# Kernel tuning notes

Hardware: AMD Instinct MI355X
Metric: run time of the kernel (lower is better)

Reference implementation:

```python
import jax, jax.numpy as jnp
import numpy as np

N, L, C, H, W, HEAD = 16, 256, 512, 32, 32, 16

def setup_inputs() -> dict:
    key = jax.random.key(0)
    ks = jax.random.split(key, 8)
    s = 0.02  # weight init scale
    return {
        "feature": jax.random.normal(ks[0], (N, C, H, W), jnp.float32),
        "token": jax.random.normal(ks[1], (N, L, C), jnp.float32),
        "wq": jax.random.normal(ks[2], (C, C), jnp.float32) * s,
        "bq": jax.random.normal(ks[3], (C,), jnp.float32) * s,
        "wk": jax.random.normal(ks[4], (C, C), jnp.float32) * s,
        "bk": jax.random.normal(ks[5], (C,), jnp.float32) * s,
        "wv": jax.random.normal(ks[6], (C, C), jnp.float32) * s,
        "bv": jax.random.normal(ks[7], (C,), jnp.float32) * s,
    }

def reference(feature, token, wq, bq, wk, bk, wv, bv):
    n, c, hgt, wid = feature.shape
    h = HEAD
    d = c // h
    l = token.shape[1]
    scale = jnp.asarray(np.sqrt(c / h), feature.dtype)
    tok = token.transpose(0, 2, 1)  # (N, C, L)
    # 1x1 conv projections == per-position GEMMs
    v = (jnp.einsum('ncl,dc->ndl', tok, wv) + bv[None, :, None]).reshape(n, h, d, l)
    k = (jnp.einsum('ncl,dc->ndl', tok, wk) + bk[None, :, None]).reshape(n, h, d, l)
    q = (jnp.einsum('nchw,dc->ndhw', feature, wq) + bq[None, :, None, None])
    q = q.reshape(n, h, d, hgt * wid).transpose(0, 1, 3, 2)  # (N, h, HW, d)
    scores = jnp.einsum('nhqd,nhdl->nhql', q, k) / scale  # (N, h, HW, L)
    coef = jax.nn.softmax(scores, axis=-1)
    proj = jnp.einsum('nhdl,nhql->nhdq', v, coef)  # (N, h, d, HW)
    return feature + proj.reshape(n, c, hgt, wid)
```

## Files before the change

### kernel.cpp

```cpp
#include <hip/hip_runtime.h>
#include <hip/hip_bf16.h>

#define N_ 16
#define L_ 256
#define C_ 512
#define HW_ 1024
#define HEADS_ 16
#define DH_ 32

typedef unsigned short u16;
typedef unsigned int u32;
typedef __attribute__((ext_vector_type(8))) short short8_t;
typedef __attribute__((ext_vector_type(4))) float f32x4;

__device__ __forceinline__ u16 f2bs(float f) {
    union { float f; u32 i; } x; x.f = f;
    u32 r = x.i + 0x7fffu + ((x.i >> 16) & 1u);
    return (u16)(r >> 16);
}
__device__ __forceinline__ u32 cvt_pk_bf16(float lo, float hi) {
    u32 r;
    asm("v_cvt_pk_bf16_f32 %0, %1, %2" : "=v"(r) : "v"(lo), "v"(hi));
    return r;
}
__device__ __forceinline__ void cvt8(const float* __restrict__ src, void* dst) {
    float4 lo = *(const float4*)src;
    float4 hi = *(const float4*)(src + 4);
    union { u32 w[4]; short8_t v; } pk;
    pk.w[0] = cvt_pk_bf16(lo.x, lo.y);
    pk.w[1] = cvt_pk_bf16(lo.z, lo.w);
    pk.w[2] = cvt_pk_bf16(hi.x, hi.y);
    pk.w[3] = cvt_pk_bf16(hi.z, hi.w);
    *(short8_t*)dst = pk.v;
}
#define AS1(p) (const __attribute__((address_space(1))) void*)(p)
#define AS3(p) (__attribute__((address_space(3))) void*)(p)

__global__ __launch_bounds__(256) void prep_kernel(
    const float* __restrict__ feature, const float* __restrict__ token,
    const float* __restrict__ wk, const float* __restrict__ wv,
    const float* __restrict__ bk, const float* __restrict__ bv,
    u16* __restrict__ Ftb, u16* __restrict__ Kout, u16* __restrict__ Vt)
{
    __shared__ __align__(16) unsigned char smem[32768];
    const int t = threadIdx.x;

    if (blockIdx.x < 256) {
        const int kvid = blockIdx.x;
        const int xcd = kvid & 7, j = kvid >> 3;
        const int m0 = (xcd * 4 + (j & 3)) * 128;
        const int n0 = (j >> 2) * 64;
        const int lane = t & 63, wid = t >> 6;
        const int i16 = lane & 15, g = lane >> 4;
        const int wm = wid >> 1, wn = wid & 1;
        const int r8 = t >> 3, c8 = t & 7;
        u16* Tok = (u16*)smem;
        u16* Bk  = (u16*)(smem + 16384);
        u16* Bv  = (u16*)(smem + 24576);
        u16 (*LTo)[72] = (u16(*)[72])smem;

        f32x4 ak[4][2], av[4][2];
        #pragma unroll
        for (int mt = 0; mt < 4; ++mt)
            #pragma unroll
            for (int nt = 0; nt < 2; ++nt) {
                ak[mt][nt] = (f32x4){0.f, 0.f, 0.f, 0.f};
                av[mt][nt] = (f32x4){0.f, 0.f, 0.f, 0.f};
            }

        for (int c0 = 0; c0 < C_; c0 += 64) {
            __syncthreads();
            #pragma unroll
            for (int p = 0; p < 4; ++p) {
                const int m = p * 32 + r8;
                cvt8(&token[(size_t)(m0 + m) * C_ + c0 + c8 * 8],
                     &Tok[m * 64 + ((c8 ^ (m & 7)) << 3)]);
            }
            #pragma unroll
            for (int p = 0; p < 2; ++p) {
                const int m = p * 32 + r8;
                const int sw = m * 64 + ((c8 ^ (m & 7)) << 3);
                cvt8(&wk[(size_t)(n0 + m) * C_ + c0 + c8 * 8], &Bk[sw]);
                cvt8(&wv[(size_t)(n0 + m) * C_ + c0 + c8 * 8], &Bv[sw]);
            }
            __syncthreads();
            #pragma unroll
            for (int ks = 0; ks < 2; ++ks) {
                short8_t a[4], bbk[2], bbv[2];
                #pragma unroll
                for (int mt = 0; mt < 4; ++mt) {
                    const int m = wm * 64 + mt * 16 + i16;
                    a[mt] = *(const short8_t*)&Tok[m * 64 + ((((ks << 2) | g) ^ (m & 7)) << 3)];
                }
                #pragma unroll
                for (int nt = 0; nt < 2; ++nt) {
                    const int d = wn * 32 + nt * 16 + i16;
                    const int sw = d * 64 + ((((ks << 2) | g) ^ (d & 7)) << 3);
                    bbk[nt] = *(const short8_t*)&Bk[sw];
                    bbv[nt] = *(const short8_t*)&Bv[sw];
                }
                #pragma unroll
                for (int mt = 0; mt < 4; ++mt)
                    #pragma unroll
                    for (int nt = 0; nt < 2; ++nt) {
                        ak[mt][nt] = __builtin_amdgcn_mfma_f32_16x16x32_bf16(
                            a[mt], bbk[nt], ak[mt][nt], 0, 0, 0);
                        av[mt][nt] = __builtin_amdgcn_mfma_f32_16x16x32_bf16(
                            a[mt], bbv[nt], av[mt][nt], 0, 0, 0);
                    }
            }
        }
        const int nb = m0 >> 8, l0 = m0 & 255;
        const size_t vtbase = (size_t)nb * C_ * L_;
        #pragma unroll
        for (int nt = 0; nt < 2; ++nt) {
            const int d = n0 + wn * 32 + nt * 16 + i16;
            const float bb = bv[d];
            #pragma unroll
            for (int mt = 0; mt < 4; ++mt) {
                ushort4 w;
                w.x = f2bs(av[mt][nt][0] + bb);
                w.y = f2bs(av[mt][nt][1] + bb);
                w.z = f2bs(av[mt][nt][2] + bb);
                w.w = f2bs(av[mt][nt][3] + bb);
                const int l = l0 + wm * 64 + mt * 16 + g * 4;
                *(ushort4*)&Vt[vtbase + (size_t)d * L_ + l] = w;
            }
        }
        __syncthreads();
        #pragma unroll
        for (int nt = 0; nt < 2; ++nt) {
            const int col = wn * 32 + nt * 16 + i16;
            const float bb = bk[n0 + col];
            #pragma unroll
            for (int mt = 0; mt < 4; ++mt)
                #pragma unroll
                for (int r = 0; r < 4; ++r)
                    LTo[wm * 64 + mt * 16 + g * 4 + r][col] = f2bs(ak[mt][nt][r] + bb);
        }
        __syncthreads();
        #pragma unroll
        for (int rep = 0; rep < 4; ++rep) {
            const int m = (t >> 3) + rep * 32;
            const int cs2 = (t & 7) * 8;
            *(short8_t*)&Kout[(size_t)(m0 + m) * C_ + n0 + cs2] = *(short8_t*)&LTo[m][cs2];
        }
    } else {
        float (*LT)[67] = (float(*)[67])smem;
        const int tidx = blockIdx.x - 256;
        const int pb = tidx & 15, cb = (tidx >> 4) & 7, n = tidx >> 7;
        const int c0 = cb * 64, pos0 = pb * 64;

        #pragma unroll
        for (int r = 0; r < 4; ++r) {
            const int c = r * 16 + (t >> 4);
            const int p = (t & 15) * 4;
            float4 v = *(const float4*)&feature[
                ((size_t)n * C_ + c0 + c) * HW_ + pos0 + p];
            LT[c][p] = v.x; LT[c][p+1] = v.y; LT[c][p+2] = v.z; LT[c][p+3] = v.w;
        }
        __syncthreads();
        #pragma unroll
        for (int rep = 0; rep < 2; ++rep) {
            const int pos = (t >> 3) + rep * 32;
            const int c = (t & 7) * 8;
            u16 tmp[8];
            #pragma unroll
            for (int j = 0; j < 8; ++j) tmp[j] = f2bs(LT[c + j][pos]);
            *(short8_t*)&Ftb[(size_t)(n * HW_ + pos0 + pos) * C_ + c0 + c] =
                *(short8_t*)tmp;
        }
    }
}

__global__ __launch_bounds__(256) void fattn_kernel(
    const float* __restrict__ feature, const u16* __restrict__ Ftb,
    const float* __restrict__ wq, const float* __restrict__ bqv,
    const u16* __restrict__ Kws, const u16* __restrict__ Vws,
    float* __restrict__ out)
{
    __shared__ __align__(16) unsigned char smem[32768];
    const u32 QB = 12288;

    const int t = threadIdx.x;
    const int wid = t >> 6, lane = t & 63;
    const int i16 = lane & 15, g = lane >> 4;
    const int h = blockIdx.x & 15;
    const int tile = blockIdx.x >> 4;
    const int n = tile >> 4, pt = tile & 15;
    const int pos0 = pt * 64;
    const size_t kbase = ((size_t)n * L_) * C_ + h * DH_;
    const size_t vbase = (size_t)n * C_ * L_ + (size_t)h * DH_ * L_;
    const size_t fbase = (size_t)(n * HW_ + pos0) * C_;
    const int q = wid * 16 + i16;

    const int r8 = t >> 3, gr = t & 7;
    f32x4 aq0 = {0.f, 0.f, 0.f, 0.f}, aq1 = {0.f, 0.f, 0.f, 0.f};

    #define FQ_STAGE(buf, c0) { \
        _Pragma("unroll") \
        for (int p = 0; p < 2; ++p) { \
            const int row = p * 32 + r8; \
            __builtin_amdgcn_global_load_lds( \
                AS1(Ftb + fbase + (size_t)row * C_ + (c0) + ((gr ^ (row & 7)) << 3)), \
                AS3(smem + (buf) * QB + (p * 32 + wid * 8) * 128), 16, 0, 0); } \
        { \
            const int wrow = t >> 3; \
            float wf[8]; \
            const float* wsrc = wq + (size_t)(h * 32 + wrow) * C_ + (c0) + (t & 7) * 8; \
            *(float4*)&wf[0] = *(const float4*)&wsrc[0]; \
            *(float4*)&wf[4] = *(const float4*)&wsrc[4]; \
            cvt8(wf, smem + (buf) * QB + 8192 + \
                 (u32)(wrow * 128 + (((t & 7) ^ (wrow & 7)) << 4))); \
        } }

    FQ_STAGE(0, 0);
    __syncthreads();
    #pragma unroll
    for (int cs = 0; cs < 8; ++cs) {
        const int cur = cs & 1;
        if (cs < 7) FQ_STAGE(cur ^ 1, (cs + 1) * 64);
        #pragma unroll
        for (int ks = 0; ks < 2; ++ks) {
            const int browq = wid * 16 + i16;
            short8_t b = *(const short8_t*)(smem + cur * QB +
                (u32)(browq * 128 + ((((ks << 2) | g) ^ (browq & 7)) << 4)));
            short8_t a0 = *(const short8_t*)(smem + cur * QB + 8192 +
                (u32)(i16 * 128 + ((((ks << 2) | g) ^ (i16 & 7)) << 4)));
            short8_t a1 = *(const short8_t*)(smem + cur * QB + 8192 +
                (u32)((16 + i16) * 128 + ((((ks << 2) | g) ^ (i16 & 7)) << 4)));
            aq0 = __builtin_amdgcn_mfma_f32_16x16x32_bf16(a0, b, aq0, 0, 0, 0);
            aq1 = __builtin_amdgcn_mfma_f32_16x16x32_bf16(a1, b, aq1, 0, 0, 0);
        }
        __syncthreads();
    }

    short8_t bq;
    {
        float4 b0 = *(const float4*)&bqv[h * 32 + g * 4];
        float4 b1 = *(const float4*)&bqv[h * 32 + 16 + g * 4];
        u32 A0 = cvt_pk_bf16(aq0[0] + b0.x, aq0[1] + b0.y);
        u32 A1 = cvt_pk_bf16(aq0[2] + b0.z, aq0[3] + b0.w);
        u32 B0 = cvt_pk_bf16(aq1[0] + b1.x, aq1[1] + b1.y);
        u32 B1 = cvt_pk_bf16(aq1[2] + b1.z, aq1[3] + b1.w);
        const int srcLo = ((g & 1) * 2) * 16 + i16;
        const int srcHi = srcLo + 16;
        u32 XA0 = (u32)__shfl((int)A0, srcLo), XA1 = (u32)__shfl((int)A1, srcLo);
        u32 XA2 = (u32)__shfl((int)A0, srcHi), XA3 = (u32)__shfl((int)A1, srcHi);
        u32 XB0 = (u32)__shfl((int)B0, srcLo), XB1 = (u32)__shfl((int)B1, srcLo);
        u32 XB2 = (u32)__shfl((int)B0, srcHi), XB3 = (u32)__shfl((int)B1, srcHi);
        union { u32 w[4]; short8_t v; } bp;
        bp.w[0] = g < 2 ? XA0 : XB0;
        bp.w[1] = g < 2 ? XA1 : XB1;
        bp.w[2] = g < 2 ? XA2 : XB2;
        bp.w[3] = g < 2 ? XA3 : XB3;
        bq = bp.v;
    }

    #pragma unroll
    for (int p = 0; p < 4; ++p) {
        const int kg = (lane & 3) ^ ((lane >> 3) & 3);
        const int kr = wid * 64 + p * 16 + (lane >> 2);
        const u16* ksrc = Kws + kbase + (size_t)kr * C_ + kg * 8;
        __builtin_amdgcn_global_load_lds(AS1(ksrc),
            AS3(smem + wid * 4096 + p * 1024), 16, 0, 0);
        const int vd = wid * 8 + p * 2 + (lane >> 5);
        const u16* vsrc = Vws + vbase + (size_t)vd * L_ + ((lane & 31) ^ (vd & 7)) * 8;
        __builtin_amdgcn_global_load_lds(AS1(vsrc),
            AS3(smem + 16384 + wid * 4096 + p * 1024), 16, 0, 0);
    }
    __syncthreads();

    const int kgr = g ^ ((i16 >> 1) & 3);
    f32x4 s[16];
    #pragma unroll
    for (int nf = 0; nf < 16; ++nf) {
        short8_t a = *(const short8_t*)(smem + (nf * 16 + i16) * 64 + kgr * 16);
        f32x4 z = {0.f, 0.f, 0.f, 0.f};
        s[nf] = __builtin_amdgcn_mfma_f32_16x16x32_bf16(a, bq, z, 0, 0, 0);
    }

    float mm[16], sm[16];
    #pragma unroll
    for (int nf = 0; nf < 16; ++nf)
        mm[nf] = fmaxf(fmaxf(s[nf][0], s[nf][1]), fmaxf(s[nf][2], s[nf][3]));
    #pragma unroll
    for (int st = 8; st >= 1; st >>= 1)
        #pragma unroll
        for (int i = 0; i < 8; ++i)
            if (i < st) mm[i] = fmaxf(mm[i], mm[i + st]);
    float m = mm[0];
    m = fmaxf(m, __shfl_xor(m, 16));
    m = fmaxf(m, __shfl_xor(m, 32));

    const float K2 = 0.25506288f;
    #pragma unroll
    for (int nf = 0; nf < 16; ++nf) {
        #pragma unroll
        for (int r = 0; r < 4; ++r) s[nf][r] = exp2f((s[nf][r] - m) * K2);
        sm[nf] = (s[nf][0] + s[nf][1]) + (s[nf][2] + s[nf][3]);
    }
    #pragma unroll
    for (int st = 8; st >= 1; st >>= 1)
        #pragma unroll
        for (int i = 0; i < 8; ++i)
            if (i < st) sm[i] += sm[i + st];
    float ssum = sm[0];
    ssum += __shfl_xor(ssum, 16);
    ssum += __shfl_xor(ssum, 32);
    const float pinv = 1.0f / ssum;

    __syncthreads();

    f32x4 o0 = {0.f, 0.f, 0.f, 0.f}, o1 = {0.f, 0.f, 0.f, 0.f};
    const int e7 = i16 & 7;

    #pragma unroll
    for (int hb = 0; hb < 2; ++hb) {
        #pragma unroll
        for (int nfp = 0; nfp < 8; ++nfp) {
            const int nf = hb * 8 + nfp;
            #pragma unroll
            for (int w = 0; w < 2; ++w) {
                u32 pw = cvt_pk_bf16(s[nf][2 * w] * pinv, s[nf][2 * w + 1] * pinv);
                const int gran = (nfp * 2 + (g >> 1)) ^ e7;
                *(u32*)(smem + q * 256 + gran * 16 + ((g & 1) * 2 + w) * 4) = pw;
            }
        }
        __syncthreads();
        #pragma unroll
        for (int ks = 0; ks < 4; ++ks) {
            short8_t pb = *(const short8_t*)(smem + q * 256 + (((ks * 4 + g) ^ e7) * 16));
            const int vg = (((hb * 4 + ks) * 4 + g) ^ e7) * 16;
            short8_t va0 = *(const short8_t*)(smem + 16384 + i16 * 512 + vg);
            short8_t va1 = *(const short8_t*)(smem + 16384 + (16 + i16) * 512 + vg);
            o0 = __builtin_amdgcn_mfma_f32_16x16x32_bf16(va0, pb, o0, 0, 0, 0);
            o1 = __builtin_amdgcn_mfma_f32_16x16x32_bf16(va1, pb, o1, 0, 0, 0);
        }
        if (hb == 0) __syncthreads();
    }

    const size_t obase = ((size_t)n * C_ + h * DH_) * HW_ + pos0 + q;
    #pragma unroll
    for (int r = 0; r < 4; ++r) {
        const size_t oa = obase + (size_t)(g * 4 + r) * HW_;
        out[oa] = feature[oa] + o0[r];
        const size_t ob = obase + (size_t)(16 + g * 4 + r) * HW_;
        out[ob] = feature[ob] + o1[r];
    }
}

extern "C" void kernel_launch(void* const* d_in, const int* in_sizes, int n_in,
                              void* d_out, int out_size, void* d_ws, size_t ws_size,
                              hipStream_t stream)
{
    const float* feature = (const float*)d_in[0];
    const float* token   = (const float*)d_in[1];
    const float* wq      = (const float*)d_in[2];
    const float* bq      = (const float*)d_in[3];
    const float* wk      = (const float*)d_in[4];
    const float* bk      = (const float*)d_in[5];
    const float* wv      = (const float*)d_in[6];
    const float* bv      = (const float*)d_in[7];
    float* out = (float*)d_out;

    u16* Ftb = (u16*)d_ws;
    u16* Kws = Ftb + (size_t)N_ * HW_ * C_;
    u16* Vws = Kws + (size_t)N_ * L_ * C_;

    prep_kernel<<<dim3(2304), 256, 0, stream>>>(feature, token, wk, wv,
                                                bk, bv, Ftb, Kws, Vws);
    fattn_kernel<<<dim3(4096), 256, 0, stream>>>(feature, Ftb, wq, bq,
                                                 Kws, Vws, out);
}
```

Before: 88.50 us.

## Process four heads per block to reuse staged feature tile across heads

Each block now computes the Q projection for four heads (128 output channels) from one staged feature tile, then loops over those heads for attention, instead of one block per head. This cuts re-reading the bf16 feature tile from global memory by a factor of four and reduces the grid from 4096 to 1024 blocks. In exchange, shared memory per block grows to 48KB and the accumulators grow to 8 MFMA tiles, which raises register pressure. The per-head attention runs serially inside the block with extra barriers, so there is less parallelism and possibly lower occupancy.

Result: slower. 119.6 us (+35.2%).

```diff
diff --git a/kernel.cpp b/kernel.cpp
--- a/kernel.cpp
+++ b/kernel.cpp
@@ -179,23 +179,23 @@
     const u16* __restrict__ Kws, const u16* __restrict__ Vws,
     float* __restrict__ out)
 {
-    __shared__ __align__(16) unsigned char smem[32768];
-    const u32 QB = 12288;
+    __shared__ __align__(16) unsigned char smem[49152];
+    const u32 QB = 24576;
 
     const int t = threadIdx.x;
     const int wid = t >> 6, lane = t & 63;
     const int i16 = lane & 15, g = lane >> 4;
-    const int h = blockIdx.x & 15;
-    const int tile = blockIdx.x >> 4;
+    const int hq = blockIdx.x & 3;
+    const int tile = blockIdx.x >> 2;
     const int n = tile >> 4, pt = tile & 15;
     const int pos0 = pt * 64;
-    const size_t kbase = ((size_t)n * L_) * C_ + h * DH_;
-    const size_t vbase = (size_t)n * C_ * L_ + (size_t)h * DH_ * L_;
     const size_t fbase = (size_t)(n * HW_ + pos0) * C_;
     const int q = wid * 16 + i16;
-
     const int r8 = t >> 3, gr = t & 7;
-    f32x4 aq0 = {0.f, 0.f, 0.f, 0.f}, aq1 = {0.f, 0.f, 0.f, 0.f};
+
+    f32x4 aq[8];
+    #pragma unroll
+    for (int i = 0; i < 8; ++i) aq[i] = (f32x4){0.f, 0.f, 0.f, 0.f};
 
     #define FQ_STAGE(buf, c0) { \
         _Pragma("unroll") \
@@ -205,13 +205,18 @@
                 AS1(Ftb + fbase + (size_t)row * C_ + (c0) + ((gr ^ (row & 7)) << 3)), \
                 AS3(smem + (buf) * QB + (p * 32 + wid * 8) * 128), 16, 0, 0); } \
         { \
-            const int wrow = t >> 3; \
-            float wf[8]; \
-            const float* wsrc = wq + (size_t)(h * 32 + wrow) * C_ + (c0) + (t & 7) * 8; \
-            *(float4*)&wf[0] = *(const float4*)&wsrc[0]; \
-            *(float4*)&wf[4] = *(const float4*)&wsrc[4]; \
-            cvt8(wf, smem + (buf) * QB + 8192 + \
-                 (u32)(wrow * 128 + (((t & 7) ^ (wrow & 7)) << 4))); \
+            const int wrow = t >> 1; \
+            const int cb0 = (t & 1) * 4; \
+            _Pragma("unroll") \
+            for (int cc = 0; cc < 4; ++cc) { \
+                const int c8 = cb0 + cc; \
+                float wf[8]; \
+                const float* wsrc = wq + (size_t)(hq * 128 + wrow) * C_ + (c0) + c8 * 8; \
+                *(float4*)&wf[0] = *(const float4*)&wsrc[0]; \
+                *(float4*)&wf[4] = *(const float4*)&wsrc[4]; \
+                cvt8(wf, smem + (buf) * QB + 8192 + \
+                     (u32)(wrow * 128 + ((c8 ^ (wrow & 7)) << 4))); \
+            } \
         } }
 
     FQ_STAGE(0, 0);
@@ -225,128 +230,141 @@
             const int browq = wid * 16 + i16;
             short8_t b = *(const short8_t*)(smem + cur * QB +
                 (u32)(browq * 128 + ((((ks << 2) | g) ^ (browq & 7)) << 4)));
-            short8_t a0 = *(const short8_t*)(smem + cur * QB + 8192 +
-                (u32)(i16 * 128 + ((((ks << 2) | g) ^ (i16 & 7)) << 4)));
-            short8_t a1 = *(const short8_t*)(smem + cur * QB + 8192 +
-                (u32)((16 + i16) * 128 + ((((ks << 2) | g) ^ (i16 & 7)) << 4)));
-            aq0 = __builtin_amdgcn_mfma_f32_16x16x32_bf16(a0, b, aq0, 0, 0, 0);
-            aq1 = __builtin_amdgcn_mfma_f32_16x16x32_bf16(a1, b, aq1, 0, 0, 0);
+            const u32 gsw = (u32)((((ks << 2) | g) ^ (i16 & 7)) << 4);
+            #pragma unroll
+            for (int hh = 0; hh < 4; ++hh) {
+                short8_t a0 = *(const short8_t*)(smem + cur * QB + 8192 +
+                    (u32)((hh * 32 + i16) * 128) + gsw);
+                short8_t a1 = *(const short8_t*)(smem + cur * QB + 8192 +
+                    (u32)((hh * 32 + 16 + i16) * 128) + gsw);
+                aq[2 * hh]     = __builtin_amdgcn_mfma_f32_16x16x32_bf16(a0, b, aq[2 * hh], 0, 0, 0);
+                aq[2 * hh + 1] = __builtin_amdgcn_mfma_f32_16x16x32_bf16(a1, b, aq[2 * hh + 1], 0, 0, 0);
+            }
         }
         __syncthreads();
     }
 
-    short8_t bq;
-    {
-        float4 b0 = *(const float4*)&bqv[h * 32 + g * 4];
-        float4 b1 = *(const float4*)&bqv[h * 32 + 16 + g * 4];
-        u32 A0 = cvt_pk_bf16(aq0[0] + b0.x, aq0[1] + b0.y);
-        u32 A1 = cvt_pk_bf16(aq0[2] + b0.z, aq0[3] + b0.w);
-        u32 B0 = cvt_pk_bf16(aq1[0] + b1.x, aq1[1] + b1.y);
-        u32 B1 = cvt_pk_bf16(aq1[2] + b1.z, aq1[3] + b1.w);
-        const int srcLo = ((g & 1) * 2) * 16 + i16;
-        const int srcHi = srcLo + 16;
-        u32 XA0 = (u32)__shfl((int)A0, srcLo), XA1 = (u32)__shfl((int)A1, srcLo);
-        u32 XA2 = (u32)__shfl((int)A0, srcHi), XA3 = (u32)__shfl((int)A1, srcHi);
-        u32 XB0 = (u32)__shfl((int)B0, srcLo), XB1 = (u32)__shfl((int)B1, srcLo);
-        u32 XB2 = (u32)__shfl((int)B0, srcHi), XB3 = (u32)__shfl((int)B1, srcHi);
-        union { u32 w[4]; short8_t v; } bp;
-        bp.w[0] = g < 2 ? XA0 : XB0;
-        bp.w[1] = g < 2 ? XA1 : XB1;
-        bp.w[2] = g < 2 ? XA2 : XB2;
-        bp.w[3] = g < 2 ? XA3 : XB3;
-        bq = bp.v;
-    }
+    const float K2 = 0.25506288f;
+    const int e7 = i16 & 7;
+    const int kgr = g ^ ((i16 >> 1) & 3);
 
     #pragma unroll
-    for (int p = 0; p < 4; ++p) {
-        const int kg = (lane & 3) ^ ((lane >> 3) & 3);
-        const int kr = wid * 64 + p * 16 + (lane >> 2);
-        const u16* ksrc = Kws + kbase + (size_t)kr * C_ + kg * 8;
-        __builtin_amdgcn_global_load_lds(AS1(ksrc),
-            AS3(smem + wid * 4096 + p * 1024), 16, 0, 0);
-        const int vd = wid * 8 + p * 2 + (lane >> 5);
-        const u16* vsrc = Vws + vbase + (size_t)vd * L_ + ((lane & 31) ^ (vd & 7)) * 8;
-        __builtin_amdgcn_global_load_lds(AS1(vsrc),
-            AS3(smem + 16384 + wid * 4096 + p * 1024), 16, 0, 0);
-    }
-    __syncthreads();
-
-    const int kgr = g ^ ((i16 >> 1) & 3);
-    f32x4 s[16];
-    #pragma unroll
-    for (int nf = 0; nf < 16; ++nf) {
-        short8_t a = *(const short8_t*)(smem + (nf * 16 + i16) * 64 + kgr * 16);
-        f32x4 z = {0.f, 0.f, 0.f, 0.f};
-        s[nf] = __builtin_amdgcn_mfma_f32_16x16x32_bf16(a, bq, z, 0, 0, 0);
-    }
-
-    float mm[16], sm[16];
-    #pragma unroll
-    for (int nf = 0; nf < 16; ++nf)
-        mm[nf] = fmaxf(fmaxf(s[nf][0], s[nf][1]), fmaxf(s[nf][2], s[nf][3]));
-    #pragma unroll
-    for (int st = 8; st >= 1; st >>= 1)
-        #pragma unroll
-        for (int i = 0; i < 8; ++i)
-            if (i < st) mm[i] = fmaxf(mm[i], mm[i + st]);
-    float m = mm[0];
-    m = fmaxf(m, __shfl_xor(m, 16));
-    m = fmaxf(m, __shfl_xor(m, 32));
-
-    const float K2 = 0.25506288f;
-    #pragma unroll
-    for (int nf = 0; nf < 16; ++nf) {
-        #pragma unroll
-        for (int r = 0; r < 4; ++r) s[nf][r] = exp2f((s[nf][r] - m) * K2);
-        sm[nf] = (s[nf][0] + s[nf][1]) + (s[nf][2] + s[nf][3]);
-    }
-    #pragma unroll
-    for (int st = 8; st >= 1; st >>= 1)
-        #pragma unroll
-        for (int i = 0; i < 8; ++i)
-            if (i < st) sm[i] += sm[i + st];
-    float ssum = sm[0];
-    ssum += __shfl_xor(ssum, 16);
-    ssum += __shfl_xor(ssum, 32);
-    const float pinv = 1.0f / ssum;
-
-    __syncthreads();
-
-    f32x4 o0 = {0.f, 0.f, 0.f, 0.f}, o1 = {0.f, 0.f, 0.f, 0.f};
-    const int e7 = i16 & 7;
-
-    #pragma unroll
-    for (int hb = 0; hb < 2; ++hb) {
-        #pragma unroll
-        for (int nfp = 0; nfp < 8; ++nfp) {
-            const int nf = hb * 8 + nfp;
-            #pragma unroll
-            for (int w = 0; w < 2; ++w) {
-                u32 pw = cvt_pk_bf16(s[nf][2 * w] * pinv, s[nf][2 * w + 1] * pinv);
-                const int gran = (nfp * 2 + (g >> 1)) ^ e7;
-                *(u32*)(smem + q * 256 + gran * 16 + ((g & 1) * 2 + w) * 4) = pw;
-            }
-        }
-        __syncthreads();
-        #pragma unroll
-        for (int ks = 0; ks < 4; ++ks) {
-            short8_t pb = *(const short8_t*)(smem + q * 256 + (((ks * 4 + g) ^ e7) * 16));
-            const int vg = (((hb * 4 + ks) * 4 + g) ^ e7) * 16;
-            short8_t va0 = *(const short8_t*)(smem + 16384 + i16 * 512 + vg);
-            short8_t va1 = *(const short8_t*)(smem + 16384 + (16 + i16) * 512 + vg);
-            o0 = __builtin_amdgcn_mfma_f32_16x16x32_bf16(va0, pb, o0, 0, 0, 0);
-            o1 = __builtin_amdgcn_mfma_f32_16x16x32_bf16(va1, pb, o1, 0, 0, 0);
-        }
-        if (hb == 0) __syncthreads();
-    }
-
-    const size_t obase = ((size_t)n * C_ + h * DH_) * HW_ + pos0 + q;
-    #pragma unroll
-    for (int r = 0; r < 4; ++r) {
-        const size_t oa = obase + (size_t)(g * 4 + r) * HW_;
-        out[oa] = feature[oa] + o0[r];
-        const size_t ob = obase + (size_t)(16 + g * 4 + r) * HW_;
-        out[ob] = feature[ob] + o1[r];
+    for (int h2 = 0; h2 < 4; ++h2) {
+        const int h = hq * 4 + h2;
+        const size_t kbase = ((size_t)n * L_) * C_ + h * DH_;
+        const size_t vbase = (size_t)n * C_ * L_ + (size_t)h * DH_ * L_;
+
+        short8_t bq;
+        {
+            float4 b0 = *(const float4*)&bqv[h * 32 + g * 4];
+            float4 b1 = *(const float4*)&bqv[h * 32 + 16 + g * 4];
+            u32 A0 = cvt_pk_bf16(aq[2 * h2][0] + b0.x, aq[2 * h2][1] + b0.y);
+            u32 A1 = cvt_pk_bf16(aq[2 * h2][2] + b0.z, aq[2 * h2][3] + b0.w);
+            u32 B0 = cvt_pk_bf16(aq[2 * h2 + 1][0] + b1.x, aq[2 * h2 + 1][1] + b1.y);
+            u32 B1 = cvt_pk_bf16(aq[2 * h2 + 1][2] + b1.z, aq[2 * h2 + 1][3] + b1.w);
+            const int srcLo = ((g & 1) * 2) * 16 + i16;
+            const int srcHi = srcLo + 16;
+            u32 XA0 = (u32)__shfl((int)A0, srcLo), XA1 = (u32)__shfl((int)A1, srcLo);
+            u32 XA2 = (u32)__shfl((int)A0, srcHi), XA3 = (u32)__shfl((int)A1, srcHi);
+            u32 XB0 = (u32)__shfl((int)B0, srcLo), XB1 = (u32)__shfl((int)B1, srcLo);
+            u32 XB2 = (u32)__shfl((int)B0, srcHi), XB3 = (u32)__shfl((int)B1, srcHi);
+            union { u32 w[4]; short8_t v; } bp;
+            bp.w[0] = g < 2 ? XA0 : XB0;
+            bp.w[1] = g < 2 ? XA1 : XB1;
+            bp.w[2] = g < 2 ? XA2 : XB2;
+            bp.w[3] = g < 2 ? XA3 : XB3;
+            bq = bp.v;
+        }
+
+        __syncthreads();
+        #pragma unroll
+        for (int p = 0; p < 4; ++p) {
+            const int kg = (lane & 3) ^ ((lane >> 3) & 3);
+            const int kr = wid * 64 + p * 16 + (lane >> 2);
+            const u16* ksrc = Kws + kbase + (size_t)kr * C_ + kg * 8;
+            __builtin_amdgcn_global_load_lds(AS1(ksrc),
+                AS3(smem + wid * 4096 + p * 1024), 16, 0, 0);
+            const int vd = wid * 8 + p * 2 + (lane >> 5);
+            const u16* vsrc = Vws + vbase + (size_t)vd * L_ + ((lane & 31) ^ (vd & 7)) * 8;
+            __builtin_amdgcn_global_load_lds(AS1(vsrc),
+                AS3(smem + 16384 + wid * 4096 + p * 1024), 16, 0, 0);
+        }
+        __syncthreads();
+
+        f32x4 s[16];
+        #pragma unroll
+        for (int nf = 0; nf < 16; ++nf) {
+            short8_t a = *(const short8_t*)(smem + (nf * 16 + i16) * 64 + kgr * 16);
+            f32x4 z = {0.f, 0.f, 0.f, 0.f};
+            s[nf] = __builtin_amdgcn_mfma_f32_16x16x32_bf16(a, bq, z, 0, 0, 0);
+        }
+
+        float mm[16], sm[16];
+        #pragma unroll
+        for (int nf = 0; nf < 16; ++nf)
+            mm[nf] = fmaxf(fmaxf(s[nf][0], s[nf][1]), fmaxf(s[nf][2], s[nf][3]));
+        #pragma unroll
+        for (int st = 8; st >= 1; st >>= 1)
+            #pragma unroll
+            for (int i = 0; i < 8; ++i)
+                if (i < st) mm[i] = fmaxf(mm[i], mm[i + st]);
+        float m = mm[0];
+        m = fmaxf(m, __shfl_xor(m, 16));
+        m = fmaxf(m, __shfl_xor(m, 32));
+
+        #pragma unroll
+        for (int nf = 0; nf < 16; ++nf) {
+            #pragma unroll
+            for (int r = 0; r < 4; ++r) s[nf][r] = exp2f((s[nf][r] - m) * K2);
+            sm[nf] = (s[nf][0] + s[nf][1]) + (s[nf][2] + s[nf][3]);
+        }
+        #pragma unroll
+        for (int st = 8; st >= 1; st >>= 1)
+            #pragma unroll
+            for (int i = 0; i < 8; ++i)
+                if (i < st) sm[i] += sm[i + st];
+        float ssum = sm[0];
+        ssum += __shfl_xor(ssum, 16);
+        ssum += __shfl_xor(ssum, 32);
+        const float pinv = 1.0f / ssum;
+
+        __syncthreads();
+
+        f32x4 o0 = {0.f, 0.f, 0.f, 0.f}, o1 = {0.f, 0.f, 0.f, 0.f};
+
+        #pragma unroll
+        for (int hb = 0; hb < 2; ++hb) {
+            #pragma unroll
+            for (int nfp = 0; nfp < 8; ++nfp) {
+                const int nf = hb * 8 + nfp;
+                #pragma unroll
+                for (int w = 0; w < 2; ++w) {
+                    u32 pw = cvt_pk_bf16(s[nf][2 * w] * pinv, s[nf][2 * w + 1] * pinv);
+                    const int gran = (nfp * 2 + (g >> 1)) ^ e7;
+                    *(u32*)(smem + q * 256 + gran * 16 + ((g & 1) * 2 + w) * 4) = pw;
+                }
+            }
+            __syncthreads();
+            #pragma unroll
+            for (int ks = 0; ks < 4; ++ks) {
+                short8_t pb = *(const short8_t*)(smem + q * 256 + (((ks * 4 + g) ^ e7) * 16));
+                const int vg = (((hb * 4 + ks) * 4 + g) ^ e7) * 16;
+                short8_t va0 = *(const short8_t*)(smem + 16384 + i16 * 512 + vg);
+                short8_t va1 = *(const short8_t*)(smem + 16384 + (16 + i16) * 512 + vg);
+                o0 = __builtin_amdgcn_mfma_f32_16x16x32_bf16(va0, pb, o0, 0, 0, 0);
+                o1 = __builtin_amdgcn_mfma_f32_16x16x32_bf16(va1, pb, o1, 0, 0, 0);
+            }
+            if (hb == 0) __syncthreads();
+        }
+
+        const size_t obase = ((size_t)n * C_ + h * DH_) * HW_ + pos0 + q;
+        #pragma unroll
+        for (int r = 0; r < 4; ++r) {
+            const size_t oa = obase + (size_t)(g * 4 + r) * HW_;
+            out[oa] = feature[oa] + o0[r];
+            const size_t ob = obase + (size_t)(16 + g * 4 + r) * HW_;
+            out[ob] = feature[ob] + o1[r];
+        }
     }
 }
 
@@ -370,6 +388,6 @@
 
     prep_kernel<<<dim3(2304), 256, 0, stream>>>(feature, token, wk, wv,
                                                 bk, bv, Ftb, Kws, Vws);
-    fattn_kernel<<<dim3(4096), 256, 0, stream>>>(feature, Ftb, wq, bq,
+    fattn_kernel<<<dim3(1024), 256, 0, stream>>>(feature, Ftb, wq, bq,
                                                  Kws, Vws, out);
 }
```

## Split Q projection into dedicated GEMM kernel with full-width tiles

Applied to the files above, without the earlier changes.

Replaces the bf16 feature-transpose pass and the per-head Q projection inside the attention kernel with a separate qproj kernel. Each block there computes all 512 output channels for 64 positions from a bf16 copy of wq staged in LDS, and converts and transposes the feature tile on the fly. The aim is to stop each attention block from re-reading the full feature row and wq slice for its own head. The cost is an extra kernel launch and a round trip of Q through global memory. The bf16 wq copy is stored as scratch in the output buffer at a fixed offset, which relies on the attention kernel overwriting it later.

Result: faster. 78.94 us (-10.8%).

```diff
diff --git a/kernel.cpp b/kernel.cpp
--- a/kernel.cpp
+++ b/kernel.cpp
@@ -37,10 +37,10 @@
 #define AS3(p) (__attribute__((address_space(3))) void*)(p)
 
 __global__ __launch_bounds__(256) void prep_kernel(
-    const float* __restrict__ feature, const float* __restrict__ token,
+    const float* __restrict__ token, const float* __restrict__ wq,
     const float* __restrict__ wk, const float* __restrict__ wv,
     const float* __restrict__ bk, const float* __restrict__ bv,
-    u16* __restrict__ Ftb, u16* __restrict__ Kout, u16* __restrict__ Vt)
+    u16* __restrict__ wqb, u16* __restrict__ Kout, u16* __restrict__ Vt)
 {
     __shared__ __align__(16) unsigned char smem[32768];
     const int t = threadIdx.x;
@@ -146,116 +146,122 @@
             *(short8_t*)&Kout[(size_t)(m0 + m) * C_ + n0 + cs2] = *(short8_t*)&LTo[m][cs2];
         }
     } else {
-        float (*LT)[67] = (float(*)[67])smem;
-        const int tidx = blockIdx.x - 256;
-        const int pb = tidx & 15, cb = (tidx >> 4) & 7, n = tidx >> 7;
-        const int c0 = cb * 64, pos0 = pb * 64;
-
-        #pragma unroll
-        for (int r = 0; r < 4; ++r) {
-            const int c = r * 16 + (t >> 4);
-            const int p = (t & 15) * 4;
-            float4 v = *(const float4*)&feature[
-                ((size_t)n * C_ + c0 + c) * HW_ + pos0 + p];
-            LT[c][p] = v.x; LT[c][p+1] = v.y; LT[c][p+2] = v.z; LT[c][p+3] = v.w;
-        }
+        const int idx = (blockIdx.x - 256) * 256 + t;
+        float4 v = ((const float4*)wq)[idx];
+        ushort4 w;
+        w.x = f2bs(v.x); w.y = f2bs(v.y); w.z = f2bs(v.z); w.w = f2bs(v.w);
+        ((ushort4*)wqb)[idx] = w;
+    }
+}
+
+__global__ __launch_bounds__(512) void qproj_kernel(
+    const float* __restrict__ feature, const u16* __restrict__ wqb,
+    const float* __restrict__ bq, u16* __restrict__ Qout)
+{
+    __shared__ __align__(16) unsigned char smem[149504];
+    const u32 FB = 131072;
+
+    const int t = threadIdx.x;
+    const int wv = t >> 6, lane = t & 63;
+    const int i16 = lane & 15, g = lane >> 4;
+    const int pt = blockIdx.x;
+    const int n = pt >> 4, pos0 = (pt & 15) * 64;
+    const int fr = t >> 3;
+    const int fp8 = (t & 7) * 8;
+
+    f32x4 acc[4][4];
+    #pragma unroll
+    for (int mt = 0; mt < 4; ++mt)
+        #pragma unroll
+        for (int nt = 0; nt < 4; ++nt)
+            acc[mt][nt] = (f32x4){0.f, 0.f, 0.f, 0.f};
+
+    #define QP_STAGE(buf, cs) { \
+        _Pragma("unroll") \
+        for (int p = 0; p < 8; ++p) { \
+            const int gi = p * 512 + t; \
+            const int row = gi >> 3, g8 = gi & 7; \
+            __builtin_amdgcn_global_load_lds( \
+                AS1(wqb + (size_t)row * C_ + (cs) * 64 + ((g8 ^ (row & 7)) << 3)), \
+                AS3(smem + (buf) * 65536 + gi * 16), 16, 0, 0); } \
+        { \
+            float f8[8]; \
+            const float* src = &feature[((size_t)n * C_ + (cs) * 64 + fr) * HW_ + pos0 + fp8]; \
+            *(float4*)&f8[0] = *(const float4*)&src[0]; \
+            *(float4*)&f8[4] = *(const float4*)&src[4]; \
+            u16* fb = (u16*)(smem + FB + (buf) * 9216); \
+            _Pragma("unroll") \
+            for (int jj = 0; jj < 8; ++jj) \
+                fb[(fp8 + jj) * 72 + fr] = f2bs(f8[jj]); \
+        } }
+
+    #define QP_COMPUTE(buf) { \
+        const u16* wqs = (const u16*)(smem + (buf) * 65536); \
+        const u16* fts = (const u16*)(smem + FB + (buf) * 9216); \
+        _Pragma("unroll") \
+        for (int ks = 0; ks < 2; ++ks) { \
+            short8_t a[4], b[4]; \
+            _Pragma("unroll") \
+            for (int mt = 0; mt < 4; ++mt) { \
+                const int d = wv * 64 + mt * 16 + i16; \
+                a[mt] = *(const short8_t*)&wqs[d * 64 + ((((ks << 2) | g) ^ (d & 7)) << 3)]; } \
+            _Pragma("unroll") \
+            for (int nt = 0; nt < 4; ++nt) { \
+                const int pos = nt * 16 + i16; \
+                b[nt] = *(const short8_t*)&fts[pos * 72 + ks * 32 + g * 8]; } \
+            _Pragma("unroll") \
+            for (int mt = 0; mt < 4; ++mt) \
+                _Pragma("unroll") \
+                for (int nt = 0; nt < 4; ++nt) \
+                    acc[mt][nt] = __builtin_amdgcn_mfma_f32_16x16x32_bf16( \
+                        a[mt], b[nt], acc[mt][nt], 0, 0, 0); } }
+
+    QP_STAGE(0, 0);
+    __syncthreads();
+    #pragma unroll
+    for (int cs = 0; cs < 8; ++cs) {
+        const int cur = cs & 1;
+        if (cs < 7) QP_STAGE(cur ^ 1, cs + 1);
+        QP_COMPUTE(cur);
         __syncthreads();
-        #pragma unroll
-        for (int rep = 0; rep < 2; ++rep) {
-            const int pos = (t >> 3) + rep * 32;
-            const int c = (t & 7) * 8;
-            u16 tmp[8];
-            #pragma unroll
-            for (int j = 0; j < 8; ++j) tmp[j] = f2bs(LT[c + j][pos]);
-            *(short8_t*)&Ftb[(size_t)(n * HW_ + pos0 + pos) * C_ + c0 + c] =
-                *(short8_t*)tmp;
-        }
-    }
-}
-
-__global__ __launch_bounds__(256) void fattn_kernel(
-    const float* __restrict__ feature, const u16* __restrict__ Ftb,
-    const float* __restrict__ wq, const float* __restrict__ bqv,
-    const u16* __restrict__ Kws, const u16* __restrict__ Vws,
+    }
+
+    #pragma unroll
+    for (int mt = 0; mt < 4; ++mt) {
+        const int dbase = wv * 64 + mt * 16 + g * 4;
+        float4 b4 = *(const float4*)&bq[dbase];
+        #pragma unroll
+        for (int nt = 0; nt < 4; ++nt) {
+            const int pos = nt * 16 + i16;
+            ushort4 w;
+            w.x = f2bs(acc[mt][nt][0] + b4.x);
+            w.y = f2bs(acc[mt][nt][1] + b4.y);
+            w.z = f2bs(acc[mt][nt][2] + b4.z);
+            w.w = f2bs(acc[mt][nt][3] + b4.w);
+            *(ushort4*)&Qout[(size_t)(n * HW_ + pos0 + pos) * C_ + dbase] = w;
+        }
+    }
+}
+
+__global__ __launch_bounds__(256) void attn_kernel(
+    const u16* __restrict__ Qws, const u16* __restrict__ Kws,
+    const u16* __restrict__ Vws, const float* __restrict__ feature,
     float* __restrict__ out)
 {
     __shared__ __align__(16) unsigned char smem[32768];
-    const u32 QB = 12288;
 
     const int t = threadIdx.x;
     const int wid = t >> 6, lane = t & 63;
     const int i16 = lane & 15, g = lane >> 4;
-    const int h = blockIdx.x & 15;
-    const int tile = blockIdx.x >> 4;
-    const int n = tile >> 4, pt = tile & 15;
+    const int pt = blockIdx.x, h = blockIdx.y, n = blockIdx.z;
     const int pos0 = pt * 64;
+    const size_t qbase = ((size_t)n * HW_ + pos0) * C_ + h * DH_;
     const size_t kbase = ((size_t)n * L_) * C_ + h * DH_;
     const size_t vbase = (size_t)n * C_ * L_ + (size_t)h * DH_ * L_;
-    const size_t fbase = (size_t)(n * HW_ + pos0) * C_;
+
     const int q = wid * 16 + i16;
 
-    const int r8 = t >> 3, gr = t & 7;
-    f32x4 aq0 = {0.f, 0.f, 0.f, 0.f}, aq1 = {0.f, 0.f, 0.f, 0.f};
-
-    #define FQ_STAGE(buf, c0) { \
-        _Pragma("unroll") \
-        for (int p = 0; p < 2; ++p) { \
-            const int row = p * 32 + r8; \
-            __builtin_amdgcn_global_load_lds( \
-                AS1(Ftb + fbase + (size_t)row * C_ + (c0) + ((gr ^ (row & 7)) << 3)), \
-                AS3(smem + (buf) * QB + (p * 32 + wid * 8) * 128), 16, 0, 0); } \
-        { \
-            const int wrow = t >> 3; \
-            float wf[8]; \
-            const float* wsrc = wq + (size_t)(h * 32 + wrow) * C_ + (c0) + (t & 7) * 8; \
-            *(float4*)&wf[0] = *(const float4*)&wsrc[0]; \
-            *(float4*)&wf[4] = *(const float4*)&wsrc[4]; \
-            cvt8(wf, smem + (buf) * QB + 8192 + \
-                 (u32)(wrow * 128 + (((t & 7) ^ (wrow & 7)) << 4))); \
-        } }
-
-    FQ_STAGE(0, 0);
-    __syncthreads();
-    #pragma unroll
-    for (int cs = 0; cs < 8; ++cs) {
-        const int cur = cs & 1;
-        if (cs < 7) FQ_STAGE(cur ^ 1, (cs + 1) * 64);
-        #pragma unroll
-        for (int ks = 0; ks < 2; ++ks) {
-            const int browq = wid * 16 + i16;
-            short8_t b = *(const short8_t*)(smem + cur * QB +
-                (u32)(browq * 128 + ((((ks << 2) | g) ^ (browq & 7)) << 4)));
-            short8_t a0 = *(const short8_t*)(smem + cur * QB + 8192 +
-                (u32)(i16 * 128 + ((((ks << 2) | g) ^ (i16 & 7)) << 4)));
-            short8_t a1 = *(const short8_t*)(smem + cur * QB + 8192 +
-                (u32)((16 + i16) * 128 + ((((ks << 2) | g) ^ (i16 & 7)) << 4)));
-            aq0 = __builtin_amdgcn_mfma_f32_16x16x32_bf16(a0, b, aq0, 0, 0, 0);
-            aq1 = __builtin_amdgcn_mfma_f32_16x16x32_bf16(a1, b, aq1, 0, 0, 0);
-        }
-        __syncthreads();
-    }
-
-    short8_t bq;
-    {
-        float4 b0 = *(const float4*)&bqv[h * 32 + g * 4];
-        float4 b1 = *(const float4*)&bqv[h * 32 + 16 + g * 4];
-        u32 A0 = cvt_pk_bf16(aq0[0] + b0.x, aq0[1] + b0.y);
-        u32 A1 = cvt_pk_bf16(aq0[2] + b0.z, aq0[3] + b0.w);
-        u32 B0 = cvt_pk_bf16(aq1[0] + b1.x, aq1[1] + b1.y);
-        u32 B1 = cvt_pk_bf16(aq1[2] + b1.z, aq1[3] + b1.w);
-        const int srcLo = ((g & 1) * 2) * 16 + i16;
-        const int srcHi = srcLo + 16;
-        u32 XA0 = (u32)__shfl((int)A0, srcLo), XA1 = (u32)__shfl((int)A1, srcLo);
-        u32 XA2 = (u32)__shfl((int)A0, srcHi), XA3 = (u32)__shfl((int)A1, srcHi);
-        u32 XB0 = (u32)__shfl((int)B0, srcLo), XB1 = (u32)__shfl((int)B1, srcLo);
-        u32 XB2 = (u32)__shfl((int)B0, srcHi), XB3 = (u32)__shfl((int)B1, srcHi);
-        union { u32 w[4]; short8_t v; } bp;
-        bp.w[0] = g < 2 ? XA0 : XB0;
-        bp.w[1] = g < 2 ? XA1 : XB1;
-        bp.w[2] = g < 2 ? XA2 : XB2;
-        bp.w[3] = g < 2 ? XA3 : XB3;
-        bq = bp.v;
-    }
+    short8_t bq = *(const short8_t*)&Qws[qbase + (size_t)q * C_ + g * 8];
 
     #pragma unroll
     for (int p = 0; p < 4; ++p) {
@@ -364,12 +370,14 @@
     const float* bv      = (const float*)d_in[7];
     float* out = (float*)d_out;
 
-    u16* Ftb = (u16*)d_ws;
-    u16* Kws = Ftb + (size_t)N_ * HW_ * C_;
+    u16* Qws = (u16*)d_ws;
+    u16* Kws = Qws + (size_t)N_ * HW_ * C_;
     u16* Vws = Kws + (size_t)N_ * L_ * C_;
 
-    prep_kernel<<<dim3(2304), 256, 0, stream>>>(feature, token, wk, wv,
-                                                bk, bv, Ftb, Kws, Vws);
-    fattn_kernel<<<dim3(4096), 256, 0, stream>>>(feature, Ftb, wq, bq,
-                                                 Kws, Vws, out);
-}
+    u16* wqb = (u16*)((char*)d_out + (21u << 20));
+
+    prep_kernel<<<dim3(512), 256, 0, stream>>>(token, wq, wk, wv, bk, bv,
+                                               wqb, Kws, Vws);
+    qproj_kernel<<<dim3(256), 512, 0, stream>>>(feature, wqb, bq, Qws);
+    attn_kernel<<<dim3(16, 16, 16), 256, 0, stream>>>(Qws, Kws, Vws, feature, out);
+}
```
